# Kernel optimization log

Hardware: AMD Instinct MI355X
Metric: run time of the kernel (lower is better)

## Reference

```python
import jax, jax.numpy as jnp
import numpy as np

E, H, I, K, T = 8, 1024, 2816, 2, 2048


def setup_inputs() -> dict:
    key = jax.random.key(0)
    k1, k2, k3, k4, k5, k6 = jax.random.split(key, 6)
    hidden_states = jax.random.normal(k1, (T, H), dtype=jnp.float32)
    top_k_indices = jax.random.randint(k2, (T, K), 0, E, dtype=jnp.int32)
    raw = jax.random.uniform(k3, (T, K), dtype=jnp.float32) + 0.1
    top_k_values = raw / jnp.sum(raw, axis=-1, keepdims=True)  # router softmax-like weights
    scale = 1.0 / np.sqrt(H)
    w_gate = jax.random.normal(k4, (E, H, I), dtype=jnp.float32) * scale
    w_up = jax.random.normal(k5, (E, H, I), dtype=jnp.float32) * scale
    w_down = jax.random.normal(k6, (E, I, H), dtype=jnp.float32) * (1.0 / np.sqrt(I))
    return {
        "hidden_states": hidden_states,
        "top_k_indices": top_k_indices,
        "top_k_values": top_k_values,
        "w_gate": w_gate,
        "w_up": w_up,
        "w_down": w_down,
    }


def reference(hidden_states, top_k_indices, top_k_values, w_gate, w_up, w_down):
    # Each expert: SwiGLU FFN  down( silu(x @ gate) * (x @ up) )
    # Run every expert on every token (dense reference for grouped-GEMM dispatch),
    # then combine with the per-token top-k routing weights.
    def expert(wg, wu, wd):
        g = jnp.matmul(hidden_states, wg)          # [T, I]
        u = jnp.matmul(hidden_states, wu)          # [T, I]
        return jnp.matmul(jax.nn.silu(g) * u, wd)  # [T, H]

    y = jax.vmap(expert)(w_gate, w_up, w_down)     # [E, T, H]

    t = hidden_states.shape[0]
    # comb[t, e] = sum over k of top_k_values[t, k] where top_k_indices[t, k] == e
    comb = jnp.zeros((t, w_gate.shape[0]), dtype=hidden_states.dtype)
    comb = comb.at[jnp.arange(t)[:, None], top_k_indices].add(top_k_values)
    out = jnp.einsum('te,eth->th', comb, y)        # weighted combine -> [T, H]
    return out
```

## Files before the change

kernel.cpp:

```cpp
#include <hip/hip_runtime.h>
#include <stdint.h>

#define T_TOK 2048
#define KTOP  2
#define NEXP  8
#define HDIM  1024
#define IDIM  2816

#define NPAIR 4096

#define BM        128
#define MAX_TILES 40
#define NPP       (NPAIR + BM)
#define BN2       128
#define BK2       32
#define BN3       64
#define BK3       64

#define R1BM   256
#define R1T    24
#define R1NPP  (NPAIR + R1BM)
#define R1BN2  128
#define R1BK2  32
#define R1BKp2 40
#define R1BN3  64
#define R1BK3  64
#define R1BKp3 72

typedef __attribute__((ext_vector_type(8))) short short8;
typedef __attribute__((ext_vector_type(4))) float floatx4;

__device__ __forceinline__ unsigned short f2bf(float f) {
  unsigned int u = __float_as_uint(f);
  u += 0x7fffu + ((u >> 16) & 1u);
  return (unsigned short)(u >> 16);
}

__device__ __forceinline__ void glds16(const unsigned short* g, unsigned short* l) {
  __builtin_amdgcn_global_load_lds(
      (const __attribute__((address_space(1))) unsigned int*)g,
      (__attribute__((address_space(3))) unsigned int*)l, 16, 0, 0);
}

__global__ void setup_kernel(const int* __restrict__ idx,
                             const float* __restrict__ vals,
                             int* __restrict__ hdr,
                             int* __restrict__ stok,
                             float* __restrict__ sw, int bm) {
  __shared__ int cnt[NEXP];
  __shared__ int off[NEXP];
  int tid = threadIdx.x;
  if (tid < NEXP) cnt[tid] = 0;
  __syncthreads();
  for (int p = tid; p < NPAIR; p += blockDim.x) atomicAdd(&cnt[idx[p]], 1);
  __syncthreads();
  if (tid == 0) {
    int s = 0, nt = 0;
    for (int e = 0; e < NEXP; ++e) {
      off[e] = s;
      int n = cnt[e];
      for (int t0 = 0; t0 < n; t0 += bm) {
        hdr[nt] = e;
        hdr[64 + nt] = s + t0;
        hdr[128 + nt] = s + n;
        nt++;
      }
      s += n;
    }
    for (; nt < 64; ++nt) hdr[nt] = -1;
  }
  __syncthreads();
  for (int p = tid; p < NPAIR; p += blockDim.x) {
    int e = idx[p];
    int pos = atomicAdd(&off[e], 1);
    stok[pos] = p / KTOP;
    sw[pos] = vals[p];
  }
}

__global__ void gather_kernel(const float* __restrict__ hidden,
                              const int* __restrict__ stok,
                              unsigned short* __restrict__ Xs) {
  int p = blockIdx.x;
  int t = stok[p];
  const float4* src = reinterpret_cast<const float4*>(hidden + (size_t)t * HDIM);
  float4 v = src[threadIdx.x];
  uint2 q;
  q.x = f2bf(v.x) | ((unsigned)f2bf(v.y) << 16);
  q.y = f2bf(v.z) | ((unsigned)f2bf(v.w) << 16);
  *reinterpret_cast<uint2*>(Xs + (size_t)p * HDIM + threadIdx.x * 4) = q;
}

__global__ __launch_bounds__(256) void convert_kernel(
    const float* __restrict__ wg, const float* __restrict__ wu,
    const float* __restrict__ wd, unsigned short* __restrict__ wgT,
    unsigned short* __restrict__ wuT, unsigned short* __restrict__ wdT,
    int zoff) {
  __shared__ float ls[64][65];
  int z = blockIdx.z + zoff;
  int e = blockIdx.y;
  int M = (z == 2) ? IDIM : HDIM;
  int N = (z == 2) ? HDIM : IDIM;
  const float* src = (z == 0 ? wg : z == 1 ? wu : wd) + (size_t)e * M * N;
  unsigned short* dst = (z == 0 ? wgT : z == 1 ? wuT : wdT) + (size_t)e * M * N;
  int ntx = N >> 6;
  int n0 = (blockIdx.x % ntx) << 6;
  int m0 = (blockIdx.x / ntx) << 6;
  int t = threadIdx.x;
  int rr = t >> 4, cc = (t & 15) * 4;
#pragma unroll
  for (int i = 0; i < 4; ++i) {
    int r = rr + i * 16;
    float4 v = *reinterpret_cast<const float4*>(src + (size_t)(m0 + r) * N + n0 + cc);
    ls[r][cc] = v.x; ls[r][cc + 1] = v.y; ls[r][cc + 2] = v.z; ls[r][cc + 3] = v.w;
  }
  __syncthreads();
#pragma unroll
  for (int i = 0; i < 4; ++i) {
    int n = rr + i * 16;
    uint2 q;
    q.x = f2bf(ls[cc][n])     | ((unsigned)f2bf(ls[cc + 1][n]) << 16);
    q.y = f2bf(ls[cc + 2][n]) | ((unsigned)f2bf(ls[cc + 3][n]) << 16);
    *reinterpret_cast<uint2*>(dst + (size_t)(n0 + n) * M + m0 + cc) = q;
  }
}

__global__ __launch_bounds__(256, 2) void gateup_kernel(
    const unsigned short* __restrict__ Xs, const unsigned short* __restrict__ wgT,
    const unsigned short* __restrict__ wuT, const int* __restrict__ hdr,
    const float* __restrict__ sw_g, unsigned short* __restrict__ Act) {
  int by = blockIdx.y;
  int e = hdr[by];
  if (e < 0) return;
  int row0 = hdr[64 + by];
  int rowlim = hdr[128 + by] - row0;
  int n0 = blockIdx.x * BN2;

  __shared__ __align__(16) unsigned short As[BM * BK2];
  __shared__ __align__(16) unsigned short Bg[BN2 * BK2];
  __shared__ __align__(16) unsigned short Bu[BN2 * BK2];
  __shared__ float sw[BM];

  int tid = threadIdx.x, lane = tid & 63, wave = tid >> 6;
  if (tid < BM) sw[tid] = sw_g[row0 + tid];

  const unsigned short* wgb = wgT + (size_t)e * IDIM * HDIM;
  const unsigned short* wub = wuT + (size_t)e * IDIM * HDIM;

  floatx4 accg[4][4], accu[4][4];
  floatx4 zz = {0.f, 0.f, 0.f, 0.f};
#pragma unroll
  for (int a = 0; a < 4; ++a)
#pragma unroll
    for (int b = 0; b < 4; ++b) { accg[a][b] = zz; accu[a][b] = zz; }

  int wm = (wave >> 1) * 64, wn = (wave & 1) * 64;
  int lr = lane >> 2;
  int lk = (lane & 3) * 8;
  int fr = lane & 15, fq = (lane >> 4) * 8;

  for (int kb = 0; kb < HDIM; kb += BK2) {
#pragma unroll
    for (int it = 0; it < 2; ++it) {
      int c = wave * 2 + it;
      glds16(Xs  + (size_t)(row0 + c * 16 + lr) * HDIM + kb + lk, &As[c * 512]);
      glds16(wgb + (size_t)(n0  + c * 16 + lr) * HDIM + kb + lk, &Bg[c * 512]);
      glds16(wub + (size_t)(n0  + c * 16 + lr) * HDIM + kb + lk, &Bu[c * 512]);
    }
    __syncthreads();

    short8 af[4], bg8[4], bu8[4];
#pragma unroll
    for (int x = 0; x < 4; ++x) {
      af[x]  = *reinterpret_cast<const short8*>(&As[(wm + x * 16 + fr) * BK2 + fq]);
      bg8[x] = *reinterpret_cast<const short8*>(&Bg[(wn + x * 16 + fr) * BK2 + fq]);
      bu8[x] = *reinterpret_cast<const short8*>(&Bu[(wn + x * 16 + fr) * BK2 + fq]);
    }
#pragma unroll
    for (int tm = 0; tm < 4; ++tm)
#pragma unroll
      for (int tn = 0; tn < 4; ++tn) {
        accg[tm][tn] = __builtin_amdgcn_mfma_f32_16x16x32_bf16(af[tm], bg8[tn], accg[tm][tn], 0, 0, 0);
        accu[tm][tn] = __builtin_amdgcn_mfma_f32_16x16x32_bf16(af[tm], bu8[tn], accu[tm][tn], 0, 0, 0);
      }
    __syncthreads();
  }

#pragma unroll
  for (int tm = 0; tm < 4; ++tm)
#pragma unroll
    for (int tn = 0; tn < 4; ++tn)
#pragma unroll
      for (int r = 0; r < 4; ++r) {
        int rl = wm + tm * 16 + (lane >> 4) * 4 + r;
        if (rl < rowlim) {
          int col = n0 + wn + tn * 16 + fr;
          float g = accg[tm][tn][r];
          float u = accu[tm][tn][r];
          float s = g / (1.f + __expf(-g));
          Act[(size_t)(row0 + rl) * IDIM + col] = f2bf(s * u * sw[rl]);
        }
      }
}

__global__ __launch_bounds__(256, 3) void down_kernel(
    const unsigned short* __restrict__ Act, const unsigned short* __restrict__ wdT,
    const int* __restrict__ hdr, const int* __restrict__ stok,
    float* __restrict__ out) {
  int by = blockIdx.y;
  int e = hdr[by];
  if (e < 0) return;
  int row0 = hdr[64 + by];
  int rowlim = hdr[128 + by] - row0;
  int n0 = blockIdx.x * BN3;

  __shared__ __align__(16) unsigned short As[BM * BK3];
  __shared__ __align__(16) unsigned short Bd[BN3 * BK3];
  __shared__ int stk[BM];

  int tid = threadIdx.x, lane = tid & 63, wave = tid >> 6;
  if (tid < BM) stk[tid] = stok[row0 + tid];

  const unsigned short* wdb = wdT + (size_t)e * HDIM * IDIM;

  floatx4 acc[4][2];
  floatx4 zz = {0.f, 0.f, 0.f, 0.f};
#pragma unroll
  for (int a = 0; a < 4; ++a) { acc[a][0] = zz; acc[a][1] = zz; }

  int wm = (wave >> 1) * 64, wn = (wave & 1) * 32;
  int lr8 = lane >> 3;
  int lk8 = (lane & 7) * 8;
  int fr = lane & 15, fq = (lane >> 4) * 8;

  for (int kb = 0; kb < IDIM; kb += BK3) {
#pragma unroll
    for (int it = 0; it < 4; ++it) {
      int c = wave * 4 + it;
      glds16(Act + (size_t)(row0 + c * 8 + lr8) * IDIM + kb + lk8, &As[c * 512]);
    }
#pragma unroll
    for (int it = 0; it < 2; ++it) {
      int c = wave * 2 + it;
      glds16(wdb + (size_t)(n0 + c * 8 + lr8) * IDIM + kb + lk8, &Bd[c * 512]);
    }
    __syncthreads();

#pragma unroll
    for (int ks = 0; ks < BK3; ks += 32) {
      short8 af[4], bd8[2];
#pragma unroll
      for (int x = 0; x < 4; ++x)
        af[x] = *reinterpret_cast<const short8*>(&As[(wm + x * 16 + fr) * BK3 + ks + fq]);
#pragma unroll
      for (int x = 0; x < 2; ++x)
        bd8[x] = *reinterpret_cast<const short8*>(&Bd[(wn + x * 16 + fr) * BK3 + ks + fq]);
#pragma unroll
      for (int tm = 0; tm < 4; ++tm)
#pragma unroll
        for (int tn = 0; tn < 2; ++tn)
          acc[tm][tn] = __builtin_amdgcn_mfma_f32_16x16x32_bf16(af[tm], bd8[tn], acc[tm][tn], 0, 0, 0);
    }
    __syncthreads();
  }

#pragma unroll
  for (int tm = 0; tm < 4; ++tm)
#pragma unroll
    for (int tn = 0; tn < 2; ++tn)
#pragma unroll
      for (int r = 0; r < 4; ++r) {
        int rl = wm + tm * 16 + (lane >> 4) * 4 + r;
        if (rl < rowlim) {
          int col = n0 + wn + tn * 16 + fr;
          unsafeAtomicAdd(&out[(size_t)stk[rl] * HDIM + col], acc[tm][tn][r]);
        }
      }
}

__global__ __launch_bounds__(512, 2) void gateup_fb(
    const unsigned short* __restrict__ Xs, const float* __restrict__ wg,
    const float* __restrict__ wu, const int* __restrict__ hdr,
    const float* __restrict__ sw_g, unsigned short* __restrict__ Act) {
  int by = blockIdx.y;
  int e = hdr[by];
  if (e < 0) return;
  int row0 = hdr[64 + by];
  int row_end = hdr[128 + by];
  int n0 = blockIdx.x * R1BN2;

  __shared__ __align__(16) unsigned short As[R1BM * R1BKp2];
  __shared__ __align__(16) unsigned short Bg[R1BN2 * R1BKp2];
  __shared__ __align__(16) unsigned short Bu[R1BN2 * R1BKp2];
  __shared__ float sw[R1BM];

  int tid = threadIdx.x, lane = tid & 63, wave = tid >> 6;
  if (tid < R1BM) sw[tid] = sw_g[row0 + tid];

  const float* wgb = wg + (size_t)e * HDIM * IDIM;
  const float* wub = wu + (size_t)e * HDIM * IDIM;

  floatx4 accg[4][4], accu[4][4];
  floatx4 zz = {0.f, 0.f, 0.f, 0.f};
#pragma unroll
  for (int a = 0; a < 4; ++a)
#pragma unroll
    for (int b = 0; b < 4; ++b) { accg[a][b] = zz; accu[a][b] = zz; }

  int wm = (wave >> 1) * 64, wn = (wave & 1) * 64;

  for (int kb = 0; kb < HDIM; kb += R1BK2) {
    __syncthreads();
#pragma unroll
    for (int it = 0; it < 2; ++it) {
      int cc = wave * 2 + it;
      int m = cc * 16 + (lane >> 2);
      int k = (lane & 3) * 8;
      uint4 v = *reinterpret_cast<const uint4*>(Xs + (size_t)(row0 + m) * HDIM + kb + k);
      *reinterpret_cast<uint4*>(&As[m * R1BKp2 + k]) = v;
    }
#pragma unroll
    for (int it = 0; it < 2; ++it) {
      int cc = wave * 2 + it;
      const float* wb = (cc & 8) ? wub : wgb;
      unsigned short* Bs = (cc & 8) ? Bu : Bg;
      int r = cc & 7;
      int kblk = r >> 1, nh = r & 1;
      int n = nh * 64 + lane;
      int k = kblk * 8;
      const float* src = wb + (size_t)(kb + k) * IDIM + n0 + n;
      uint4 q;
      q.x = f2bf(src[0])                | ((unsigned)f2bf(src[(size_t)IDIM])     << 16);
      q.y = f2bf(src[2 * (size_t)IDIM]) | ((unsigned)f2bf(src[3 * (size_t)IDIM]) << 16);
      q.z = f2bf(src[4 * (size_t)IDIM]) | ((unsigned)f2bf(src[5 * (size_t)IDIM]) << 16);
      q.w = f2bf(src[6 * (size_t)IDIM]) | ((unsigned)f2bf(src[7 * (size_t)IDIM]) << 16);
      *reinterpret_cast<uint4*>(&Bs[n * R1BKp2 + k]) = q;
    }
    __syncthreads();

    int krd = (lane >> 4) * 8;
    short8 af[4], bgf[4], buf_[4];
#pragma unroll
    for (int tm = 0; tm < 4; ++tm)
      af[tm] = *reinterpret_cast<const short8*>(&As[(wm + tm * 16 + (lane & 15)) * R1BKp2 + krd]);
#pragma unroll
    for (int tn = 0; tn < 4; ++tn) {
      bgf[tn]  = *reinterpret_cast<const short8*>(&Bg[(wn + tn * 16 + (lane & 15)) * R1BKp2 + krd]);
      buf_[tn] = *reinterpret_cast<const short8*>(&Bu[(wn + tn * 16 + (lane & 15)) * R1BKp2 + krd]);
    }
#pragma unroll
    for (int tm = 0; tm < 4; ++tm)
#pragma unroll
      for (int tn = 0; tn < 4; ++tn) {
        accg[tm][tn] = __builtin_amdgcn_mfma_f32_16x16x32_bf16(af[tm], bgf[tn], accg[tm][tn], 0, 0, 0);
        accu[tm][tn] = __builtin_amdgcn_mfma_f32_16x16x32_bf16(af[tm], buf_[tn], accu[tm][tn], 0, 0, 0);
      }
  }

  int rowlim = row_end - row0;
#pragma unroll
  for (int tm = 0; tm < 4; ++tm)
#pragma unroll
    for (int tn = 0; tn < 4; ++tn)
#pragma unroll
      for (int r = 0; r < 4; ++r) {
        int rl = wm + tm * 16 + (lane >> 4) * 4 + r;
        if (rl < rowlim) {
          int col = n0 + wn + tn * 16 + (lane & 15);
          float g = accg[tm][tn][r];
          float u = accu[tm][tn][r];
          float s = g / (1.f + __expf(-g));
          Act[(size_t)(row0 + rl) * IDIM + col] = f2bf(s * u * sw[rl]);
        }
      }
}

__global__ __launch_bounds__(512, 2) void down_fb(
    const unsigned short* __restrict__ Act, const float* __restrict__ wd,
    const int* __restrict__ hdr, const int* __restrict__ stok,
    float* __restrict__ out) {
  int by = blockIdx.y;
  int e = hdr[by];
  if (e < 0) return;
  int row0 = hdr[64 + by];
  int row_end = hdr[128 + by];
  int n0 = blockIdx.x * R1BN3;

  __shared__ __align__(16) unsigned short As[R1BM * R1BKp3];
  __shared__ __align__(16) unsigned short Bd[R1BN3 * R1BKp3];
  __shared__ int stk[R1BM];

  int tid = threadIdx.x, lane = tid & 63, wave = tid >> 6;
  if (tid < R1BM) stk[tid] = stok[row0 + tid];

  const float* wdb = wd + (size_t)e * IDIM * HDIM;

  floatx4 acc[4][2];
  floatx4 zz = {0.f, 0.f, 0.f, 0.f};
#pragma unroll
  for (int a = 0; a < 4; ++a) { acc[a][0] = zz; acc[a][1] = zz; }

  int wm = (wave >> 1) * 64, wn = (wave & 1) * 32;

  for (int kb = 0; kb < IDIM; kb += R1BK3) {
    __syncthreads();
#pragma unroll
    for (int it = 0; it < 4; ++it) {
      int cc = wave * 4 + it;
      int m = cc * 8 + (lane >> 3);
      int k = (lane & 7) * 8;
      uint4 v = *reinterpret_cast<const uint4*>(Act + (size_t)(row0 + m) * IDIM + kb + k);
      *reinterpret_cast<uint4*>(&As[m * R1BKp3 + k]) = v;
    }
    {
      int n = lane;
      int k = wave * 8;
      const float* src = wdb + (size_t)(kb + k) * HDIM + n0 + n;
      uint4 q;
      q.x = f2bf(src[0])        | ((unsigned)f2bf(src[HDIM])     << 16);
      q.y = f2bf(src[2 * HDIM]) | ((unsigned)f2bf(src[3 * HDIM]) << 16);
      q.z = f2bf(src[4 * HDIM]) | ((unsigned)f2bf(src[5 * HDIM]) << 16);
      q.w = f2bf(src[6 * HDIM]) | ((unsigned)f2bf(src[7 * HDIM]) << 16);
      *reinterpret_cast<uint4*>(&Bd[n * R1BKp3 + k]) = q;
    }
    __syncthreads();

#pragma unroll
    for (int ks = 0; ks < R1BK3; ks += 32) {
      int krd = ks + (lane >> 4) * 8;
      short8 af[4], bdf[2];
#pragma unroll
      for (int tm = 0; tm < 4; ++tm)
        af[tm] = *reinterpret_cast<const short8*>(&As[(wm + tm * 16 + (lane & 15)) * R1BKp3 + krd]);
#pragma unroll
      for (int tn = 0; tn < 2; ++tn)
        bdf[tn] = *reinterpret_cast<const short8*>(&Bd[(wn + tn * 16 + (lane & 15)) * R1BKp3 + krd]);
#pragma unroll
      for (int tm = 0; tm < 4; ++tm)
#pragma unroll
        for (int tn = 0; tn < 2; ++tn)
          acc[tm][tn] = __builtin_amdgcn_mfma_f32_16x16x32_bf16(af[tm], bdf[tn], acc[tm][tn], 0, 0, 0);
    }
  }

  int rowlim = row_end - row0;
#pragma unroll
  for (int tm = 0; tm < 4; ++tm)
#pragma unroll
    for (int tn = 0; tn < 2; ++tn)
#pragma unroll
      for (int r = 0; r < 4; ++r) {
        int rl = wm + tm * 16 + (lane >> 4) * 4 + r;
        if (rl < rowlim) {
          int col = n0 + wn + tn * 16 + (lane & 15);
          unsafeAtomicAdd(&out[(size_t)stk[rl] * HDIM + col], acc[tm][tn][r]);
        }
      }
}

extern "C" void kernel_launch(void* const* d_in, const int* in_sizes, int n_in,
                              void* d_out, int out_size, void* d_ws, size_t ws_size,
                              hipStream_t stream) {
  const float* hidden = (const float*)d_in[0];
  const int* idx = (const int*)d_in[1];
  const float* vals = (const float*)d_in[2];
  const float* wg = (const float*)d_in[3];
  const float* wu = (const float*)d_in[4];
  const float* wd = (const float*)d_in[5];
  float* out = (float*)d_out;
  char* ws = (char*)d_ws;

  hipMemsetAsync(d_out, 0, (size_t)out_size * sizeof(float), stream);

  const size_t OFF_STOK = 4096;
  const size_t OFF_SW   = OFF_STOK + (size_t)NPP * 4;
  const size_t OFF_XS   = 65536;
  const size_t OFF_ACT  = OFF_XS + (size_t)NPP * HDIM * 2;
  const size_t OFF_WG   = OFF_ACT + (size_t)NPP * IDIM * 2;
  const size_t WSZ      = (size_t)NEXP * HDIM * IDIM * 2;
  const size_t OFF_WU   = OFF_WG + WSZ;
  const size_t NEED     = OFF_WU + WSZ;

  if (ws_size >= NEED) {
    int* hdr = (int*)ws;
    int* stok = (int*)(ws + OFF_STOK);
    float* sw = (float*)(ws + OFF_SW);
    unsigned short* Xs  = (unsigned short*)(ws + OFF_XS);
    unsigned short* Act = (unsigned short*)(ws + OFF_ACT);
    unsigned short* wgT = (unsigned short*)(ws + OFF_WG);
    unsigned short* wuT = (unsigned short*)(ws + OFF_WU);
    unsigned short* wdT = wgT;

    setup_kernel<<<1, 256, 0, stream>>>(idx, vals, hdr, stok, sw, BM);
    convert_kernel<<<dim3(704, NEXP, 2), 256, 0, stream>>>(wg, wu, wd, wgT, wuT, wdT, 0);
    gather_kernel<<<NPAIR, 256, 0, stream>>>(hidden, stok, Xs);
    gateup_kernel<<<dim3(IDIM / BN2, MAX_TILES), 256, 0, stream>>>(Xs, wgT, wuT, hdr, sw, Act);
    convert_kernel<<<dim3(704, NEXP, 1), 256, 0, stream>>>(wg, wu, wd, wgT, wuT, wdT, 2);
    down_kernel<<<dim3(HDIM / BN3, MAX_TILES), 256, 0, stream>>>(Act, wdT, hdr, stok, out);
  } else {
    int* hdr = (int*)ws;
    int* stok = (int*)(ws + 4096);
    float* sw = (float*)(ws + 4096 + (size_t)R1NPP * 4);
    unsigned short* Xs  = (unsigned short*)(ws + 65536);
    unsigned short* Act = (unsigned short*)(ws + 65536 + (size_t)R1NPP * HDIM * 2);

    setup_kernel<<<1, 256, 0, stream>>>(idx, vals, hdr, stok, sw, R1BM);
    gather_kernel<<<NPAIR, 256, 0, stream>>>(hidden, stok, Xs);
    gateup_fb<<<dim3(IDIM / R1BN2, R1T), 512, 0, stream>>>(Xs, wg, wu, hdr, sw, Act);
    down_fb<<<dim3(HDIM / R1BN3, R1T), 512, 0, stream>>>(Act, wd, hdr, stok, out);
  }
}
```

Measured before the change: 456.3 us.

## Swizzle LDS tiles, swap grid axes, and widen transposed weight stores

```diff
diff --git a/kernel.cpp b/kernel.cpp
--- a/kernel.cpp
+++ b/kernel.cpp
@@ -115,13 +115,16 @@
     ls[r][cc] = v.x; ls[r][cc + 1] = v.y; ls[r][cc + 2] = v.z; ls[r][cc + 3] = v.w;
   }
   __syncthreads();
-#pragma unroll
-  for (int i = 0; i < 4; ++i) {
-    int n = rr + i * 16;
-    uint2 q;
-    q.x = f2bf(ls[cc][n])     | ((unsigned)f2bf(ls[cc + 1][n]) << 16);
-    q.y = f2bf(ls[cc + 2][n]) | ((unsigned)f2bf(ls[cc + 3][n]) << 16);
-    *reinterpret_cast<uint2*>(dst + (size_t)(n0 + n) * M + m0 + cc) = q;
+  int mc = (t & 7) * 8, nn = t >> 3;
+#pragma unroll
+  for (int i = 0; i < 2; ++i) {
+    int n = nn + i * 32;
+    uint4 q;
+    q.x = f2bf(ls[mc][n])     | ((unsigned)f2bf(ls[mc + 1][n]) << 16);
+    q.y = f2bf(ls[mc + 2][n]) | ((unsigned)f2bf(ls[mc + 3][n]) << 16);
+    q.z = f2bf(ls[mc + 4][n]) | ((unsigned)f2bf(ls[mc + 5][n]) << 16);
+    q.w = f2bf(ls[mc + 6][n]) | ((unsigned)f2bf(ls[mc + 7][n]) << 16);
+    *reinterpret_cast<uint4*>(dst + (size_t)(n0 + n) * M + m0 + mc) = q;
   }
 }
 
@@ -129,12 +132,12 @@
     const unsigned short* __restrict__ Xs, const unsigned short* __restrict__ wgT,
     const unsigned short* __restrict__ wuT, const int* __restrict__ hdr,
     const float* __restrict__ sw_g, unsigned short* __restrict__ Act) {
-  int by = blockIdx.y;
-  int e = hdr[by];
+  int bx = blockIdx.x;
+  int e = hdr[bx];
   if (e < 0) return;
-  int row0 = hdr[64 + by];
-  int rowlim = hdr[128 + by] - row0;
-  int n0 = blockIdx.x * BN2;
+  int row0 = hdr[64 + bx];
+  int rowlim = hdr[128 + bx] - row0;
+  int n0 = blockIdx.y * BN2;
 
   __shared__ __align__(16) unsigned short As[BM * BK2];
   __shared__ __align__(16) unsigned short Bg[BN2 * BK2];
@@ -156,8 +159,9 @@
 
   int wm = (wave >> 1) * 64, wn = (wave & 1) * 64;
   int lr = lane >> 2;
-  int lk = (lane & 3) * 8;
-  int fr = lane & 15, fq = (lane >> 4) * 8;
+  int lk = (((lane & 3) ^ ((lr >> 1) & 3)) * 8);
+  int fr = lane & 15;
+  int fq = (((lane >> 4) ^ ((fr >> 1) & 3)) * 8);
 
   for (int kb = 0; kb < HDIM; kb += BK2) {
 #pragma unroll
@@ -207,12 +211,12 @@
     const unsigned short* __restrict__ Act, const unsigned short* __restrict__ wdT,
     const int* __restrict__ hdr, const int* __restrict__ stok,
     float* __restrict__ out) {
-  int by = blockIdx.y;
-  int e = hdr[by];
+  int bx = blockIdx.x;
+  int e = hdr[bx];
   if (e < 0) return;
-  int row0 = hdr[64 + by];
-  int rowlim = hdr[128 + by] - row0;
-  int n0 = blockIdx.x * BN3;
+  int row0 = hdr[64 + bx];
+  int rowlim = hdr[128 + bx] - row0;
+  int n0 = blockIdx.y * BN3;
 
   __shared__ __align__(16) unsigned short As[BM * BK3];
   __shared__ __align__(16) unsigned short Bd[BN3 * BK3];
@@ -230,8 +234,9 @@
 
   int wm = (wave >> 1) * 64, wn = (wave & 1) * 32;
   int lr8 = lane >> 3;
-  int lk8 = (lane & 7) * 8;
-  int fr = lane & 15, fq = (lane >> 4) * 8;
+  int lk8 = (((lane & 7) ^ lr8) * 8);
+  int fr = lane & 15;
+  int fk = fr & 7;
 
   for (int kb = 0; kb < IDIM; kb += BK3) {
 #pragma unroll
@@ -248,13 +253,15 @@
 
 #pragma unroll
     for (int ks = 0; ks < BK3; ks += 32) {
+      int q8 = (ks >> 3) + (lane >> 4);
+      int fo = ((q8 ^ fk) * 8);
       short8 af[4], bd8[2];
 #pragma unroll
       for (int x = 0; x < 4; ++x)
-        af[x] = *reinterpret_cast<const short8*>(&As[(wm + x * 16 + fr) * BK3 + ks + fq]);
+        af[x] = *reinterpret_cast<const short8*>(&As[(wm + x * 16 + fr) * BK3 + fo]);
 #pragma unroll
       for (int x = 0; x < 2; ++x)
-        bd8[x] = *reinterpret_cast<const short8*>(&Bd[(wn + x * 16 + fr) * BK3 + ks + fq]);
+        bd8[x] = *reinterpret_cast<const short8*>(&Bd[(wn + x * 16 + fr) * BK3 + fo]);
 #pragma unroll
       for (int tm = 0; tm < 4; ++tm)
 #pragma unroll
@@ -494,9 +501,9 @@
     setup_kernel<<<1, 256, 0, stream>>>(idx, vals, hdr, stok, sw, BM);
     convert_kernel<<<dim3(704, NEXP, 2), 256, 0, stream>>>(wg, wu, wd, wgT, wuT, wdT, 0);
     gather_kernel<<<NPAIR, 256, 0, stream>>>(hidden, stok, Xs);
-    gateup_kernel<<<dim3(IDIM / BN2, MAX_TILES), 256, 0, stream>>>(Xs, wgT, wuT, hdr, sw, Act);
+    gateup_kernel<<<dim3(MAX_TILES, IDIM / BN2), 256, 0, stream>>>(Xs, wgT, wuT, hdr, sw, Act);
     convert_kernel<<<dim3(704, NEXP, 1), 256, 0, stream>>>(wg, wu, wd, wgT, wuT, wdT, 2);
-    down_kernel<<<dim3(HDIM / BN3, MAX_TILES), 256, 0, stream>>>(Act, wdT, hdr, stok, out);
+    down_kernel<<<dim3(MAX_TILES, HDIM / BN3), 256, 0, stream>>>(Act, wdT, hdr, stok, out);
   } else {
     int* hdr = (int*)ws;
     int* stok = (int*)(ws + 4096);
```

After: 452.9 us. About the same (-0.8%).
